# Kernel optimization log

Measured on AMD Instinct MI355X. Metric: run time of the kernel, lower is better.

Reference implementation:

```python
import jax, jax.numpy as jnp
import numpy as np
from jax import lax

B, C_IN, HC, H, W, K = 32, 32, 64, 64, 64, 3


def _conv(x, w, b):
    # x: [B,C,H,W], w: [O,I,K,K] -> [B,O,H,W] (stride 1, pad 1)
    y = lax.conv_general_dilated(x, w, window_strides=(1, 1), padding=[(1, 1), (1, 1)],
                                 dimension_numbers=("NCHW", "OIHW", "NCHW"))
    return y + b[None, :, None, None]


def setup_inputs() -> dict:
    key = jax.random.key(0)
    ks = jax.random.split(key, 20)
    d = {
        "x": jax.random.normal(ks[0], (B, C_IN, H, W), jnp.float32),
        "hidden_state": jax.random.normal(ks[1], (B, HC, H, W), jnp.float32),
        "cell_state": jax.random.normal(ks[2], (B, HC, H, W), jnp.float32),
    }
    sx = 1.0 / np.sqrt(C_IN * K * K)
    sh = 1.0 / np.sqrt(HC * K * K)
    names_x = ["w_xi", "w_xf", "w_xo", "w_xg"]
    names_h = ["w_hi", "w_hf", "w_ho", "w_hg"]
    for i, n in enumerate(names_x):
        d[n] = jax.random.uniform(ks[3 + i], (HC, C_IN, K, K), jnp.float32, -sx, sx)
        d["b" + n[1:]] = jax.random.uniform(ks[7 + i], (HC,), jnp.float32, -sx, sx)
    for i, n in enumerate(names_h):
        d[n] = jax.random.uniform(ks[11 + i], (HC, HC, K, K), jnp.float32, -sh, sh)
        d["b" + n[1:]] = jax.random.uniform(ks[15 + i], (HC,), jnp.float32, -sh, sh)
    return d


def reference(x, hidden_state, cell_state,
              w_xi, w_xf, w_xo, w_xg, b_xi, b_xf, b_xo, b_xg,
              w_hi, w_hf, w_ho, w_hg, b_hi, b_hf, b_ho, b_hg):
    Wx = jnp.concatenate([w_xi, w_xf, w_xo, w_xg], axis=0)
    bx = jnp.concatenate([b_xi, b_xf, b_xo, b_xg], axis=0)
    Wh = jnp.concatenate([w_hi, w_hf, w_ho, w_hg], axis=0)
    bh = jnp.concatenate([b_hi, b_hf, b_ho, b_hg], axis=0)
    gates = _conv(x, Wx, bx) + _conv(hidden_state, Wh, bh)  # [B,4*HC,H,W]
    zi, zf, zo, zg = jnp.split(gates, 4, axis=1)
    i = jax.nn.sigmoid(zi)
    f = jax.nn.sigmoid(zf)
    o = jax.nn.sigmoid(zo)
    g = jnp.tanh(zg)
    c_new = f * cell_state + i * g
    h_new = o * jnp.tanh(c_new)
    return (h_new, c_new)
```

## Files before the change

kernel.cpp:

```cpp
#include <hip/hip_runtime.h>


#define B_   32
#define CIN  32
#define HC_  64
#define HH   64
#define WW   64

#define A_ELEMS (9 * 8 * 6 * 64 * 8)
#define P_ROW   (12 * 66 * 8)
#define SLAB    24576

typedef __attribute__((ext_vector_type(8)))  short  short8;
typedef __attribute__((ext_vector_type(16))) float  floatx16;

struct PackArgs {
    const float* wx[4]; const float* wh[4];
    const float* bx[4]; const float* bh[4];
};

__device__ __forceinline__ short f2bf(float f) {
    unsigned u = __float_as_uint(f);
    u += 0x7FFFu + ((u >> 16) & 1u);
    return (short)(u >> 16);
}

__device__ __forceinline__ void gl_lds16(const short* g, short* l) {
    __builtin_amdgcn_global_load_lds(
        (const __attribute__((address_space(1))) unsigned int*)g,
        (__attribute__((address_space(3))) unsigned int*)l, 16, 0, 0);
}

__global__ __launch_bounds__(256) void pack_weights(PackArgs pa, short* a_pk, float* bias) {
    int idx = blockIdx.x * 256 + threadIdx.x;
    if (idx < A_ELEMS) {
        int j    = idx & 7;
        int lane = (idx >> 3) & 63;
        int rest = idx >> 9;
        int kk   = rest % 6;
        int rest2 = rest / 6;
        int s    = rest2 % 8;
        int tap  = rest2 / 8;
        int og = s >> 1, fi = s & 1;
        int m32 = lane & 31;
        int gate = 2 * fi + (m32 >> 4);
        int oc   = og * 16 + (m32 & 15);
        int c    = kk * 16 + (lane >> 5) * 8 + j;
        int ky = tap / 3, kx = tap - 3 * ky;
        float v = (c < CIN)
            ? pa.wx[gate][((oc * CIN + c) * 3 + ky) * 3 + kx]
            : pa.wh[gate][((oc * HC_ + (c - CIN)) * 3 + ky) * 3 + kx];
        a_pk[idx] = f2bf(v);
    }
    if (idx < 256) {
        int gate = idx >> 6, oc = idx & 63;
        bias[idx] = pa.bx[gate][oc] + pa.bh[gate][oc];
    }
}

__global__ __launch_bounds__(256) void pack_input(const float* __restrict__ x,
                                                  const float* __restrict__ h,
                                                  short* __restrict__ P) {
    const int yy = blockIdx.x, b = blockIdx.y;
    int4* prow4 = (int4*)(P + ((size_t)b * 66 + yy) * P_ROW);

    if (yy == 0 || yy == 65) {
        int4 z = {0, 0, 0, 0};
        for (int g = threadIdx.x; g < 792; g += 256) prow4[g] = z;
        return;
    }

    __shared__ short t[64 * 98];
    const int y = yy - 1;
    const int col = threadIdx.x & 63, cg = threadIdx.x >> 6;
    for (int c = cg; c < 96; c += 4) {
        float v = (c < CIN) ? x[((b * CIN + c) * HH + y) * WW + col]
                            : h[((b * HC_ + (c - CIN)) * HH + y) * WW + col];
        t[col * 98 + c] = f2bf(v);
    }
    __syncthreads();

    for (int g = threadIdx.x; g < 792; g += 256) {
        int pc = g / 66, xx = g - 66 * pc;
        int4 val = {0, 0, 0, 0};
        if (xx >= 1 && xx <= 64) {
            const short* sp = &t[(xx - 1) * 98 + pc * 8];
            val.x = *(const int*)(sp + 0); val.y = *(const int*)(sp + 2);
            val.z = *(const int*)(sp + 4); val.w = *(const int*)(sp + 6);
        }
        prow4[g] = val;
    }
}

__global__ __launch_bounds__(512, 4) void convlstm_main(
    const short* __restrict__ P, const short* __restrict__ a_pk,
    const float* __restrict__ bias, const float* __restrict__ cell,
    float* __restrict__ out)
{
    __shared__ __align__(16) short As[SLAB];

    const int tid = threadIdx.x;
    const int b  = blockIdx.x >> 5;
    const int y0 = (blockIdx.x & 31) * 2;

    const int wv = tid >> 6, lane = tid & 63;
    const int ln31 = lane & 31, hg = lane >> 5;
    const int og = wv & 3, nh = wv >> 2;
    const int y = y0 + nh;

    floatx16 acc[2][2];
    #pragma unroll
    for (int fi = 0; fi < 2; ++fi)
        #pragma unroll
        for (int ns = 0; ns < 2; ++ns)
            #pragma unroll
            for (int q = 0; q < 16; ++q) acc[fi][ns][q] = 0.f;

    const int a_base = og * 12 * 64 * 8 + lane * 8;
    const int lnoff  = (hg * 66 + ln31) * 8;

    for (int ky = 0; ky < 3; ++ky)
    for (int kx = 0; kx < 3; ++kx) {
        const int tap = ky * 3 + kx;
        {
            const short* slab = a_pk + tap * SLAB;
            #pragma unroll
            for (int i = 0; i < 6; ++i) {
                int id = i * 512 + tid;
                gl_lds16(slab + id * 8, As + (i * 512 + wv * 64) * 8);
            }
        }
        __syncthreads();

        const short* Brow = P + ((size_t)(b * 66) + y + ky) * P_ROW + kx * 8 + lnoff;

        #pragma unroll
        for (int kk = 0; kk < 6; ++kk) {
            short8 a0 = *(const short8*)&As[a_base + (0 * 6 + kk) * 512];
            short8 a1 = *(const short8*)&As[a_base + (1 * 6 + kk) * 512];
            short8 b0 = *(const short8*)&Brow[(2 * kk * 66 + 0 ) * 8];
            short8 b1 = *(const short8*)&Brow[(2 * kk * 66 + 32) * 8];
            acc[0][0] = __builtin_amdgcn_mfma_f32_32x32x16_bf16(a0, b0, acc[0][0], 0, 0, 0);
            acc[0][1] = __builtin_amdgcn_mfma_f32_32x32x16_bf16(a0, b1, acc[0][1], 0, 0, 0);
            acc[1][0] = __builtin_amdgcn_mfma_f32_32x32x16_bf16(a1, b0, acc[1][0], 0, 0, 0);
            acc[1][1] = __builtin_amdgcn_mfma_f32_32x32x16_bf16(a1, b1, acc[1][1], 0, 0, 0);
        }
        __syncthreads();
    }

    const size_t plane = (size_t)B_ * HC_ * HH * WW;
    #pragma unroll
    for (int q = 0; q < 4; ++q)
    #pragma unroll
    for (int b8 = 0; b8 < 2; ++b8) {
        const int oc16 = q + 4 * hg + 8 * b8;
        const int oc = og * 16 + oc16;
        const float Bi = bias[oc],       Bf = bias[64 + oc];
        const float Bo = bias[128 + oc], Bg = bias[192 + oc];
        const int r_lo = q + 4 * b8, r_hi = q + 4 * (2 + b8);
        #pragma unroll
        for (int ns = 0; ns < 2; ++ns) {
            float zi = acc[0][ns][r_lo] + Bi;
            float zf = acc[0][ns][r_hi] + Bf;
            float zo = acc[1][ns][r_lo] + Bo;
            float zg = acc[1][ns][r_hi] + Bg;
            float ig = 1.f / (1.f + __expf(-zi));
            float fg = 1.f / (1.f + __expf(-zf));
            float sg = 1.f / (1.f + __expf(-zo));
            float e2 = __expf(2.f * zg);
            float gg = 1.f - 2.f / (e2 + 1.f);
            const int x = ns * 32 + ln31;
            size_t off = ((size_t)(b * HC_ + oc) * HH + y) * WW + x;
            float cn = fg * cell[off] + ig * gg;
            float ec = __expf(2.f * cn);
            out[off] = sg * (1.f - 2.f / (ec + 1.f));
            out[plane + off] = cn;
        }
    }
}

extern "C" void kernel_launch(void* const* d_in, const int* in_sizes, int n_in,
                              void* d_out, int out_size, void* d_ws, size_t ws_size,
                              hipStream_t stream) {
    PackArgs pa;
    pa.wx[0] = (const float*)d_in[3];  pa.bx[0] = (const float*)d_in[4];
    pa.wx[1] = (const float*)d_in[5];  pa.bx[1] = (const float*)d_in[6];
    pa.wx[2] = (const float*)d_in[7];  pa.bx[2] = (const float*)d_in[8];
    pa.wx[3] = (const float*)d_in[9];  pa.bx[3] = (const float*)d_in[10];
    pa.wh[0] = (const float*)d_in[11]; pa.bh[0] = (const float*)d_in[12];
    pa.wh[1] = (const float*)d_in[13]; pa.bh[1] = (const float*)d_in[14];
    pa.wh[2] = (const float*)d_in[15]; pa.bh[2] = (const float*)d_in[16];
    pa.wh[3] = (const float*)d_in[17]; pa.bh[3] = (const float*)d_in[18];

    short* a_pk = (short*)d_ws;
    float* bias = (float*)((char*)d_ws + A_ELEMS * sizeof(short));
    short* P    = (short*)((char*)d_ws + 443392);

    pack_weights<<<dim3(A_ELEMS / 256), dim3(256), 0, stream>>>(pa, a_pk, bias);
    pack_input <<<dim3(66, B_), dim3(256), 0, stream>>>(
        (const float*)d_in[0], (const float*)d_in[1], P);
    convlstm_main<<<dim3(B_ * 32), dim3(512), 0, stream>>>(
        P, a_pk, bias, (const float*)d_in[2], (float*)d_out);
}
```

Before: 230.3 us.

## Double-buffer weight chunks in LDS to overlap loads with MFMA

Reorders the packed weight layout so each tap's K range splits into two contiguous half-chunks. The main loop now prefetches the next chunk into a second LDS buffer via global_load_lds while MFMAs consume the current one. The aim is to hide weight-load latency behind compute. LDS use stays the same (two half-size buffers), but the fully unrolled 18-step loop raises code size and register pressure, and any sync left at the loop end still serialises each step.

```diff
diff --git a/kernel.cpp b/kernel.cpp
--- a/kernel.cpp
+++ b/kernel.cpp
@@ -7,9 +7,9 @@
 #define HH   64
 #define WW   64
 
-#define A_ELEMS (9 * 8 * 6 * 64 * 8)
+#define A_ELEMS (9 * 6 * 8 * 64 * 8)
 #define P_ROW   (12 * 66 * 8)
-#define SLAB    24576
+#define CHUNK   12288
 
 typedef __attribute__((ext_vector_type(8)))  short  short8;
 typedef __attribute__((ext_vector_type(16))) float  floatx16;
@@ -37,10 +37,10 @@
         int j    = idx & 7;
         int lane = (idx >> 3) & 63;
         int rest = idx >> 9;
-        int kk   = rest % 6;
-        int rest2 = rest / 6;
-        int s    = rest2 % 8;
-        int tap  = rest2 / 8;
+        int s    = rest & 7;
+        int rest2 = rest >> 3;
+        int kk   = rest2 % 6;
+        int tap  = rest2 / 6;
         int og = s >> 1, fi = s & 1;
         int m32 = lane & 31;
         int gate = 2 * fi + (m32 >> 4);
@@ -97,7 +97,7 @@
     const float* __restrict__ bias, const float* __restrict__ cell,
     float* __restrict__ out)
 {
-    __shared__ __align__(16) short As[SLAB];
+    __shared__ __align__(16) short As[2][CHUNK];
 
     const int tid = threadIdx.x;
     const int b  = blockIdx.x >> 5;
@@ -116,30 +116,40 @@
             #pragma unroll
             for (int q = 0; q < 16; ++q) acc[fi][ns][q] = 0.f;
 
-    const int a_base = og * 12 * 64 * 8 + lane * 8;
+    const int a_base = og * 1024 + lane * 8;
     const int lnoff  = (hg * 66 + ln31) * 8;
 
-    for (int ky = 0; ky < 3; ++ky)
-    for (int kx = 0; kx < 3; ++kx) {
-        const int tap = ky * 3 + kx;
-        {
-            const short* slab = a_pk + tap * SLAB;
+    {
+        const short* src = a_pk;
+        #pragma unroll
+        for (int i = 0; i < 3; ++i)
+            gl_lds16(src + (i * 512 + tid) * 8, &As[0][(i * 512 + wv * 64) * 8]);
+    }
+    __syncthreads();
+
+    #pragma unroll
+    for (int c = 0; c < 18; ++c) {
+        const int cur = c & 1;
+        if (c < 17) {
+            const short* src = a_pk + (c + 1) * CHUNK;
             #pragma unroll
-            for (int i = 0; i < 6; ++i) {
-                int id = i * 512 + tid;
-                gl_lds16(slab + id * 8, As + (i * 512 + wv * 64) * 8);
-            }
-        }
-        __syncthreads();
-
+            for (int i = 0; i < 3; ++i)
+                gl_lds16(src + (i * 512 + tid) * 8,
+                         &As[cur ^ 1][(i * 512 + wv * 64) * 8]);
+        }
+
+        const int tap = c >> 1, half = c & 1;
+        const int ky = tap / 3, kx = tap % 3;
         const short* Brow = P + ((size_t)(b * 66) + y + ky) * P_ROW + kx * 8 + lnoff;
-
-        #pragma unroll
-        for (int kk = 0; kk < 6; ++kk) {
-            short8 a0 = *(const short8*)&As[a_base + (0 * 6 + kk) * 512];
-            short8 a1 = *(const short8*)&As[a_base + (1 * 6 + kk) * 512];
-            short8 b0 = *(const short8*)&Brow[(2 * kk * 66 + 0 ) * 8];
-            short8 b1 = *(const short8*)&Brow[(2 * kk * 66 + 32) * 8];
+        const short* Ac = As[cur];
+
+        #pragma unroll
+        for (int kkl = 0; kkl < 3; ++kkl) {
+            const int kkg = half * 3 + kkl;
+            short8 a0 = *(const short8*)&Ac[a_base + kkl * 4096];
+            short8 a1 = *(const short8*)&Ac[a_base + kkl * 4096 + 512];
+            short8 b0 = *(const short8*)&Brow[(2 * kkg * 66 + 0 ) * 8];
+            short8 b1 = *(const short8*)&Brow[(2 * kkg * 66 + 32) * 8];
             acc[0][0] = __builtin_amdgcn_mfma_f32_32x32x16_bf16(a0, b0, acc[0][0], 0, 0, 0);
             acc[0][1] = __builtin_amdgcn_mfma_f32_32x32x16_bf16(a0, b1, acc[0][1], 0, 0, 0);
             acc[1][0] = __builtin_amdgcn_mfma_f32_32x32x16_bf16(a1, b0, acc[1][0], 0, 0, 0);
```

Measured after the change: 231.8 us. No clear change (+0.6%).
